# Performance work log

Hardware: AMD Instinct MI355X
Metric: run time of the kernel (lower is better)

Reference implementation:

```python
import jax, jax.numpy as jnp
import numpy as np

N_FFT = 4096
HOP = 1024
EPS = 1e-10


def hann(n):
    # periodic Hann window, matches torch.hann_window(n)
    return 0.5 - 0.5 * jnp.cos(2.0 * jnp.pi * jnp.arange(n) / n)


def stft(x, window):
    # x: (..., T) real -> (..., F, frames) complex; center=True, reflect pad, onesided
    pad = N_FFT // 2
    x = jnp.pad(x, [(0, 0)] * (x.ndim - 1) + [(pad, pad)], mode='reflect')
    n_frames = 1 + (x.shape[-1] - N_FFT) // HOP
    idx = jnp.arange(n_frames)[:, None] * HOP + jnp.arange(N_FFT)[None, :]
    frames = x[..., idx] * window  # (..., frames, N_FFT)
    return jnp.swapaxes(jnp.fft.rfft(frames, axis=-1), -1, -2)  # (..., F, frames)


def istft(spec, window, length):
    # spec: (..., F, frames) complex -> (..., length) real; torch.istft semantics (center=True)
    frames = jnp.fft.irfft(jnp.swapaxes(spec, -1, -2), n=N_FFT, axis=-1) * window
    n_frames = frames.shape[-2]
    out_len = N_FFT + HOP * (n_frames - 1)
    idx = (jnp.arange(n_frames)[:, None] * HOP + jnp.arange(N_FFT)[None, :]).reshape(-1)
    flat = frames.reshape(frames.shape[:-2] + (-1,))
    y = jnp.zeros(frames.shape[:-2] + (out_len,), frames.dtype).at[..., idx].add(flat)
    wsq = jnp.zeros((out_len,), frames.dtype).at[idx].add(jnp.tile(window ** 2, n_frames))
    y = y / jnp.where(wsq > 1e-11, wsq, 1.0)
    pad = N_FFT // 2
    return y[..., pad:pad + length]


def setup_inputs() -> dict:
    key = jax.random.key(0)
    k1, k2, k3 = jax.random.split(key, 3)
    audio = jax.random.normal(k1, (2, 2, 441000), jnp.float32)
    W = jax.random.normal(k2, (4, 2049, 2049), jnp.float32) * 0.02
    b = jax.random.normal(k3, (4, 2049), jnp.float32) * 0.01
    return {"audio": audio, "W": W, "b": b}


def reference(audio, W, b):
    window = hann(N_FFT).astype(audio.dtype)
    mix = stft(audio, window)                 # (N, C, F, T) complex64
    X = jnp.abs(mix)                          # ComplexNorm, mono=False, power=1
    Xd = jax.lax.stop_gradient(X)             # Separator feeds X.detach() to target models
    # target models: per-target linear over frequency bins + ReLU (nonneg spectrogram)
    V = jax.nn.relu(jnp.einsum('ncft,jgf->njcgt', Xd, W) + b[None, :, None, :, None])
    # wiener(iterations=0, softmask=False, residual=False): y_j = v_j * exp(i*angle(mix))
    phase = mix / (jnp.abs(mix) + EPS)        # unit-magnitude complex
    Y = V.astype(phase.real.dtype) * phase[:, None]  # (N, J, C, F, T) complex
    estimates = istft(Y, window, audio.shape[-1])    # (N, J, C, T_audio)
    return estimates
```

## Files before the change

### kernel.cpp

```cpp
#include <hip/hip_runtime.h>
#include <hip/hip_bf16.h>
#include <math.h>

#define T_AUDIO 441000
#define NH   2048
#define HOP  1024
#define NBINS 2049
#define NFRAMES 431
#define PAD  2048

#define GP  2176
#define KP  2112
#define TPN 448

#define NBLK 108
#define SPAN 7168

#define TWO_PI 6.2831853071795864769f

#define PADI(i) ((i) + ((i) >> 4))

typedef __bf16 bf16_t;
typedef bf16_t bf16x8 __attribute__((ext_vector_type(8)));
typedef bf16_t bf16x4 __attribute__((ext_vector_type(4)));
typedef float f32x4 __attribute__((ext_vector_type(4)));
typedef _Float16 h16;
typedef h16 h16x2 __attribute__((ext_vector_type(2)));

__device__ __forceinline__ unsigned pack_bf2(float a, float b) {
    union { bf16_t h; unsigned short u; } ca, cb;
    ca.h = (bf16_t)a; cb.h = (bf16_t)b;
    return (unsigned)ca.u | ((unsigned)cb.u << 16);
}
__device__ __forceinline__ float2 unpack_bf2(unsigned v) {
    union { unsigned u; float f; } a, b;
    a.u = v << 16;
    b.u = v & 0xffff0000u;
    return make_float2(a.f, b.f);
}

__device__ __forceinline__ float2 cadd(float2 a, float2 b) { return make_float2(a.x + b.x, a.y + b.y); }
__device__ __forceinline__ float2 csub(float2 a, float2 b) { return make_float2(a.x - b.x, a.y - b.y); }
__device__ __forceinline__ float2 cmul(float2 a, float2 b) {
    return make_float2(a.x * b.x - a.y * b.y, a.x * b.y + a.y * b.x);
}
__device__ __forceinline__ float2 cmulc(float2 u, float2 w) {
    return make_float2(u.x * w.x + u.y * w.y, u.y * w.x - u.x * w.y);
}

template<bool FWD>
__device__ __forceinline__ void fft2048_reg8(float2* x, int tid,
                                             const float2* __restrict__ tw) {
    const float sgn = FWD ? -1.0f : 1.0f;
    const float R2 = 0.70710678118654752440f;
    int s = 1, ls = 0, fac = 2;
    #pragma unroll
    for (int st = 0; st < 3; st++) {
        int q = tid & (s - 1);
        int p = tid >> ls;
        int e = p * fac;
        float2 w[7];
        #pragma unroll
        for (int k = 0; k < 7; k++) w[k] = tw[e * (k + 1)];
        float2 v[8];
        #pragma unroll
        for (int k = 0; k < 8; k++) v[k] = x[PADI(tid + 256 * k)];
        __syncthreads();
        float2 s0 = cadd(v[0], v[4]), s1 = cadd(v[1], v[5]),
               s2 = cadd(v[2], v[6]), s3 = cadd(v[3], v[7]);
        float2 d0 = csub(v[0], v[4]), d1 = csub(v[1], v[5]),
               d2 = csub(v[2], v[6]), d3 = csub(v[3], v[7]);
        float2 X0, X1, X2, X3, X4, X5, X6, X7;
        {
            float2 t0 = cadd(s0, s2), t1 = csub(s0, s2);
            float2 t2 = cadd(s1, s3), t3 = csub(s1, s3);
            float2 it3 = make_float2(-sgn * t3.y, sgn * t3.x);
            X0 = cadd(t0, t2); X4 = csub(t0, t2);
            X2 = cadd(t1, it3); X6 = csub(t1, it3);
        }
        {
            float2 e0 = d0;
            float2 e1 = make_float2(R2 * (d1.x - sgn * d1.y), R2 * (sgn * d1.x + d1.y));
            float2 e2 = make_float2(-sgn * d2.y, sgn * d2.x);
            float2 e3 = make_float2(-R2 * (d3.x + sgn * d3.y), R2 * (sgn * d3.x - d3.y));
            float2 t0 = cadd(e0, e2), t1 = csub(e0, e2);
            float2 t2 = cadd(e1, e3), t3 = csub(e1, e3);
            float2 it3 = make_float2(-sgn * t3.y, sgn * t3.x);
            X1 = cadd(t0, t2); X5 = csub(t0, t2);
            X3 = cadd(t1, it3); X7 = csub(t1, it3);
        }
        int ob = q + 8 * s * p;
        x[PADI(ob)] = X0;
        float2 XX[7] = {X1, X2, X3, X4, X5, X6, X7};
        #pragma unroll
        for (int k = 0; k < 7; k++) {
            float2 u = XX[k];
            x[PADI(ob + s * (k + 1))] = FWD ? cmulc(u, w[k]) : cmul(w[k], u);
        }
        __syncthreads();
        s <<= 3; ls += 3; fac <<= 3;
    }
    {
        float2 v[8];
        #pragma unroll
        for (int k = 0; k < 8; k++) v[k] = x[PADI(tid + 256 * k)];
        __syncthreads();
        #pragma unroll
        for (int h = 0; h < 2; h++) {
            float2 c0 = v[h], c1 = v[h + 2], c2 = v[h + 4], c3 = v[h + 6];
            float2 t0 = cadd(c0, c2), t1 = csub(c0, c2);
            float2 t2 = cadd(c1, c3), t3 = csub(c1, c3);
            float2 it3 = make_float2(-sgn * t3.y, sgn * t3.x);
            int base = tid + 256 * h;
            x[PADI(base)]        = cadd(t0, t2);
            x[PADI(base + 512)]  = cadd(t1, it3);
            x[PADI(base + 1024)] = csub(t0, t2);
            x[PADI(base + 1536)] = csub(t1, it3);
        }
        __syncthreads();
    }
}

__global__ __launch_bounds__(256) void k_stft(const float* __restrict__ audio,
        bf16_t* __restrict__ Xb, unsigned* __restrict__ ph,
        const float2* __restrict__ tw) {
    __shared__ float2 buf[2176];
    int blk = blockIdx.x;
    int nc = blk / NFRAMES;
    int fr = blk - nc * NFRAMES;
    const float* a = audio + (size_t)nc * T_AUDIO;
    int tid = threadIdx.x;
    int base = fr * HOP - PAD;
    #pragma unroll
    for (int it = 0; it < 8; it++) {
        int m = tid + it * 256;
        int r0 = base + 2 * m;
        int r1 = r0 + 1;
        r0 = r0 < 0 ? -r0 : (r0 >= T_AUDIO ? 2 * T_AUDIO - 2 - r0 : r0);
        r1 = r1 < 0 ? -r1 : (r1 >= T_AUDIO ? 2 * T_AUDIO - 2 - r1 : r1);
        float4 tt = ((const float4*)tw)[m];
        float x0 = a[r0] * (0.5f - 0.5f * tt.x);
        float x1 = a[r1] * (0.5f - 0.5f * tt.z);
        buf[PADI(m)] = make_float2(x0, x1);
    }
    fft2048_reg8<true>(buf, tid, tw);
    size_t orow = ((size_t)nc * NFRAMES + fr) * KP;
    bf16_t* Xrow = Xb + ((size_t)nc * TPN + fr) * KP;
    for (int k = tid; k < NBINS; k += 256) {
        float2 Zk = buf[PADI(k & 2047)];
        float2 Zm = buf[PADI((2048 - k) & 2047)];
        float ex = 0.5f * (Zk.x + Zm.x), ey = 0.5f * (Zk.y - Zm.y);
        float ox = 0.5f * (Zk.y + Zm.y), oy = -0.5f * (Zk.x - Zm.x);
        float2 w = tw[k];
        float re = ex + w.x * ox + w.y * oy;
        float im = ey + w.x * oy - w.y * ox;
        float mag = sqrtf(re * re + im * im);
        float inv = 1.0f / (mag + 1e-10f);
        Xrow[k] = (bf16_t)mag;
        ph[orow + k] = pack_bf2(re * inv, im * inv);
    }
}

__global__ __launch_bounds__(256) void k_convW(const float* __restrict__ W,
        bf16_t* __restrict__ Wb, float2* __restrict__ tw) {
    if (blockIdx.x < 16) {
        int i = blockIdx.x * 256 + threadIdx.x;
        float s, c;
        sincosf((float)i * (TWO_PI / 4096.0f), &s, &c);
        tw[i] = make_float2(c, s);
    }
    size_t idx = (size_t)blockIdx.x * 256 + threadIdx.x;
    size_t total = (size_t)4 * GP * KP / 8;
    if (idx >= total) return;
    size_t e = idx * 8;
    int f0 = (int)(e % KP);
    size_t rem = e / KP;
    int g = (int)(rem % GP);
    int j = (int)(rem / GP);
    bf16x8 v = {};
    if (g < NBINS) {
        const float* src = W + ((size_t)j * NBINS + g) * NBINS;
        #pragma unroll
        for (int r = 0; r < 8; r++) {
            int f = f0 + r;
            v[r] = (bf16_t)(f < NBINS ? src[f] : 0.0f);
        }
    }
    *(bf16x8*)(Wb + e) = v;
}

__global__ __launch_bounds__(256) void k_gemm_mfma(const bf16_t* __restrict__ Wb,
        const float* __restrict__ bias, const bf16_t* __restrict__ Xb,
        bf16_t* __restrict__ V) {
    __shared__ bf16_t As[128 * 64];
    __shared__ bf16_t Bs[64 * 64];
    int id = blockIdx.x;
    int xcd = id & 7, nn = id >> 3;
    int G = xcd + 8 * (nn / 28);
    if (G >= 68) return;
    int m28 = nn % 28;
    int j  = G / 17;
    int g0 = (G % 17) * 128;
    int nc = m28 / 7;
    int t0 = (m28 % 7) * 64;
    const bf16_t* A = Wb + ((size_t)j * GP + g0) * KP;
    const bf16_t* B = Xb + ((size_t)nc * TPN + t0) * KP;
    int tid = threadIdx.x;
    int lane = tid & 63, wid = tid >> 6;
    int wm = wid >> 1, wn = wid & 1;

    const bf16_t* srcA[4];
    #pragma unroll
    for (int i = 0; i < 4; i++) {
        int s = i * 256 + tid;
        int r = s >> 3, cc = (s & 7) ^ (r & 7);
        srcA[i] = A + (size_t)r * KP + cc * 8;
    }
    const bf16_t* srcB[2];
    #pragma unroll
    for (int i = 0; i < 2; i++) {
        int s = i * 256 + tid;
        int r = s >> 3, cc = (s & 7) ^ (r & 7);
        srcB[i] = B + (size_t)r * KP + cc * 8;
    }

    int laneLo = lane & 15, laneHi = lane >> 4;
    int offA[4][2], offB[2][2];
    #pragma unroll
    for (int mm = 0; mm < 4; mm++) {
        int r = wm * 64 + mm * 16 + laneLo;
        #pragma unroll
        for (int kk = 0; kk < 2; kk++) {
            int c = kk * 4 + laneHi;
            offA[mm][kk] = r * 128 + ((c ^ (r & 7)) << 4);
        }
    }
    #pragma unroll
    for (int n = 0; n < 2; n++) {
        int r = wn * 32 + n * 16 + laneLo;
        #pragma unroll
        for (int kk = 0; kk < 2; kk++) {
            int c = kk * 4 + laneHi;
            offB[n][kk] = r * 128 + ((c ^ (r & 7)) << 4);
        }
    }

    f32x4 acc[4][2];
    #pragma unroll
    for (int mm = 0; mm < 4; mm++)
        #pragma unroll
        for (int n = 0; n < 2; n++)
            acc[mm][n] = (f32x4){0.f, 0.f, 0.f, 0.f};

    for (int k0 = 0; k0 < KP; k0 += 64) {
        #pragma unroll
        for (int i = 0; i < 4; i++)
            __builtin_amdgcn_global_load_lds(
                (const __attribute__((address_space(1))) void*)(srcA[i] + k0),
                (__attribute__((address_space(3))) void*)(As + (i * 256 + tid) * 8),
                16, 0, 0);
        #pragma unroll
        for (int i = 0; i < 2; i++)
            __builtin_amdgcn_global_load_lds(
                (const __attribute__((address_space(1))) void*)(srcB[i] + k0),
                (__attribute__((address_space(3))) void*)(Bs + (i * 256 + tid) * 8),
                16, 0, 0);
        __syncthreads();

        bf16x8 af[4][2], bfr[2][2];
        #pragma unroll
        for (int mm = 0; mm < 4; mm++)
            #pragma unroll
            for (int kk = 0; kk < 2; kk++)
                af[mm][kk] = *(const bf16x8*)((const char*)As + offA[mm][kk]);
        #pragma unroll
        for (int n = 0; n < 2; n++)
            #pragma unroll
            for (int kk = 0; kk < 2; kk++)
                bfr[n][kk] = *(const bf16x8*)((const char*)Bs + offB[n][kk]);
        #pragma unroll
        for (int mm = 0; mm < 4; mm++)
            #pragma unroll
            for (int n = 0; n < 2; n++)
                #pragma unroll
                for (int kk = 0; kk < 2; kk++)
                    acc[mm][n] = __builtin_amdgcn_mfma_f32_16x16x32_bf16(
                        af[mm][kk], bfr[n][kk], acc[mm][n], 0, 0, 0);
        __syncthreads();
    }

    int jnc = j * 4 + nc;
    int colT = laneLo;
    int rowB = laneHi * 4;
    #pragma unroll
    for (int n = 0; n < 2; n++) {
        int t = t0 + wn * 32 + n * 16 + colT;
        if (t >= NFRAMES) continue;
        size_t vrow = ((size_t)jnc * NFRAMES + t) * KP;
        #pragma unroll
        for (int mm = 0; mm < 4; mm++) {
            int g = g0 + wm * 64 + mm * 16 + rowB;
            if (g + 3 < NBINS) {
                bf16x4 o;
                #pragma unroll
                for (int r = 0; r < 4; r++)
                    o[r] = (bf16_t)fmaxf(acc[mm][n][r] + bias[j * NBINS + g + r], 0.0f);
                *(bf16x4*)(V + vrow + g) = o;
            } else {
                #pragma unroll
                for (int r = 0; r < 4; r++) {
                    int gg = g + r;
                    if (gg < NBINS)
                        V[vrow + gg] = (bf16_t)fmaxf(acc[mm][n][r] + bias[j * NBINS + gg], 0.0f);
                }
            }
        }
    }
}

__global__ __launch_bounds__(256) void k_istft(const bf16_t* __restrict__ V,
        const unsigned* __restrict__ ph, const float2* __restrict__ tw,
        h16* __restrict__ strips) {
    __shared__ float2 buf[2176];
    int b = blockIdx.x, njc = blockIdx.y;
    int n = njc >> 3, j = (njc >> 1) & 3, c = njc & 1;
    int nc = n * 2 + c;
    int jnc = j * 4 + nc;
    int tid = threadIdx.x;
    const float scale = 1.0f / 2048.0f;
    float2 acc[14];
    #pragma unroll
    for (int u = 0; u < 14; u++) acc[u] = make_float2(0.f, 0.f);

    #pragma unroll
    for (int p = 0; p < 4; p++) {
        int fr = b * 4 + p;
        if (fr < NFRAMES) {
            size_t vrow = ((size_t)jnc * NFRAMES + fr) * KP;
            size_t prow = ((size_t)nc * NFRAMES + fr) * KP;
            #pragma unroll
            for (int it = 0; it < 8; it++) {
                int k = tid + it * 256;
                int km = 2048 - k;
                float vk = (float)V[vrow + k];
                float2 pk = unpack_bf2(ph[prow + k]);
                float vm = (float)V[vrow + km];
                float2 pm = unpack_bf2(ph[prow + km]);
                float2 Yk = make_float2(vk * pk.x, vk * pk.y);
                float2 Ym = make_float2(vm * pm.x, vm * pm.y);
                float ex = 0.5f * (Yk.x + Ym.x), ey = 0.5f * (Yk.y - Ym.y);
                float wx = 0.5f * (Yk.x - Ym.x), wy = 0.5f * (Yk.y + Ym.y);
                float2 w = tw[k];
                float ox_ = w.x * wx - w.y * wy;
                float oy_ = w.x * wy + w.y * wx;
                buf[PADI(k)] = make_float2(ex - oy_, ey + ox_);
            }
            fft2048_reg8<false>(buf, tid, tw);
            #pragma unroll
            for (int it = 0; it < 8; it++) {
                int m = tid + it * 256;
                float2 z = buf[PADI(m)];
                float4 tt = ((const float4*)tw)[m];
                acc[2 * p + it].x += z.x * scale * (0.5f - 0.5f * tt.x);
                acc[2 * p + it].y += z.y * scale * (0.5f - 0.5f * tt.z);
            }
        }
    }
    h16* dst = strips + ((size_t)njc * NBLK + b) * SPAN;
    #pragma unroll
    for (int u = 0; u < 14; u++) {
        h16x2 o = { (h16)acc[u].x, (h16)acc[u].y };
        *(h16x2*)(dst + 512 * u + 2 * tid) = o;
    }
}

__global__ __launch_bounds__(256) void k_final(const h16* __restrict__ strips,
        const float2* __restrict__ tw, float* __restrict__ out) {
    int gidx = blockIdx.x * 256 + threadIdx.x;
    int t = gidx * 2;
    if (t >= T_AUDIO) return;
    int njc = blockIdx.y;
    const h16* S = strips + (size_t)njc * NBLK * SPAN;
    float o[2];
    #pragma unroll
    for (int u = 0; u < 2; u++) {
        int tt = t + u;
        int q = tt + PAD;
        int b1 = q >> 12, o1 = q & 4095;
        float s = 0.f;
        if (b1 < NBLK) s += (float)S[b1 * SPAN + o1];
        if (b1 > 0 && o1 < SPAN - 4096) s += (float)S[(b1 - 1) * SPAN + o1 + 4096];
        float wsq;
        if (tt >= 1024 && tt <= 439295) {
            wsq = 1.5f;
        } else {
            wsq = 0.f;
            int ib = q >> 10;
            #pragma unroll
            for (int d = 0; d < 4; d++) {
                int i = ib - d;
                if (i >= 0 && i < NFRAMES) {
                    int m = q - (i << 10);
                    float w = 0.5f - 0.5f * tw[m].x;
                    wsq += w * w;
                }
            }
            if (!(wsq > 1e-11f)) wsq = 1.f;
        }
        o[u] = s / wsq;
    }
    *(float2*)(out + (size_t)njc * T_AUDIO + t) = make_float2(o[0], o[1]);
}

extern "C" void kernel_launch(void* const* d_in, const int* in_sizes, int n_in,
                              void* d_out, int out_size, void* d_ws, size_t ws_size,
                              hipStream_t stream) {
    const float* audio = (const float*)d_in[0];
    const float* Wm    = (const float*)d_in[1];
    const float* bias  = (const float*)d_in[2];
    float* out = (float*)d_out;
    char* ws = (char*)d_ws;

    size_t szWb  = (size_t)4 * GP * KP * sizeof(bf16_t);
    size_t szXb  = (size_t)4 * TPN * KP * sizeof(bf16_t);
    size_t szPh  = (size_t)4 * NFRAMES * KP * sizeof(unsigned);
    size_t szV   = (size_t)16 * NFRAMES * KP * sizeof(bf16_t);
    size_t szStr = (size_t)16 * NBLK * SPAN * sizeof(h16);
    size_t szTw  = (size_t)4096 * sizeof(float2);

    bf16_t*   Wb    = (bf16_t*)ws;   ws += szWb;
    bf16_t*   Xb    = (bf16_t*)ws;   ws += szXb;
    unsigned* ph    = (unsigned*)ws; ws += szPh;
    bf16_t*   V     = (bf16_t*)ws;   ws += szV;
    h16*      strips= (h16*)ws;      ws += szStr;
    float2*   tw    = (float2*)ws;   ws += szTw;
    if ((size_t)(ws - (char*)d_ws) > ws_size) return;

    hipMemsetAsync(Xb, 0, szXb, stream);

    k_convW<<<dim3((unsigned)((4ull * GP * KP / 8 + 255) / 256)), 256, 0, stream>>>(Wm, Wb, tw);
    k_stft<<<dim3(4 * NFRAMES), 256, 0, stream>>>(audio, Xb, ph, tw);
    k_gemm_mfma<<<dim3(72 * 28), 256, 0, stream>>>(Wb, bias, Xb, V);
    k_istft<<<dim3(NBLK, 16), 256, 0, stream>>>(V, ph, tw, strips);
    k_final<<<dim3((T_AUDIO / 2 + 255) / 256, 16), 256, 0, stream>>>(strips, tw, out);
}
```

Before: 243.9 us.

## Double-buffer GEMM LDS tiles and merge STFT with weight conversion kernel

```diff
diff --git a/kernel.cpp b/kernel.cpp
--- a/kernel.cpp
+++ b/kernel.cpp
@@ -12,9 +12,13 @@
 #define GP  2176
 #define KP  2112
 #define TPN 448
+#define NKT (KP / 64)
 
 #define NBLK 108
 #define SPAN 7168
+
+#define NSTFT (4 * NFRAMES)
+#define NCONV ((4 * GP * KP / 8 + 255) / 256)
 
 #define TWO_PI 6.2831853071795864769f
 
@@ -46,6 +50,15 @@
 }
 __device__ __forceinline__ float2 cmulc(float2 u, float2 w) {
     return make_float2(u.x * w.x + u.y * w.y, u.y * w.x - u.x * w.y);
+}
+
+__global__ void k_tab(float2* __restrict__ tw) {
+    int i = blockIdx.x * 256 + threadIdx.x;
+    if (i < 4096) {
+        float s, c;
+        sincosf((float)i * (TWO_PI / 4096.0f), &s, &c);
+        tw[i] = make_float2(c, s);
+    }
 }
 
 template<bool FWD>
@@ -121,15 +134,37 @@
     }
 }
 
-__global__ __launch_bounds__(256) void k_stft(const float* __restrict__ audio,
+__global__ __launch_bounds__(256) void k_prep(const float* __restrict__ audio,
+        const float* __restrict__ W, bf16_t* __restrict__ Wb,
         bf16_t* __restrict__ Xb, unsigned* __restrict__ ph,
         const float2* __restrict__ tw) {
     __shared__ float2 buf[2176];
-    int blk = blockIdx.x;
-    int nc = blk / NFRAMES;
-    int fr = blk - nc * NFRAMES;
+    int bid = blockIdx.x;
+    int tid = threadIdx.x;
+    if (bid >= NSTFT) {
+        size_t idx = (size_t)(bid - NSTFT) * 256 + tid;
+        size_t total = (size_t)4 * GP * KP / 8;
+        if (idx >= total) return;
+        size_t e = idx * 8;
+        int f0 = (int)(e % KP);
+        size_t rem = e / KP;
+        int g = (int)(rem % GP);
+        int j = (int)(rem / GP);
+        bf16x8 v = {};
+        if (g < NBINS) {
+            const float* src = W + ((size_t)j * NBINS + g) * NBINS;
+            #pragma unroll
+            for (int r = 0; r < 8; r++) {
+                int f = f0 + r;
+                v[r] = (bf16_t)(f < NBINS ? src[f] : 0.0f);
+            }
+        }
+        *(bf16x8*)(Wb + e) = v;
+        return;
+    }
+    int nc = bid / NFRAMES;
+    int fr = bid - nc * NFRAMES;
     const float* a = audio + (size_t)nc * T_AUDIO;
-    int tid = threadIdx.x;
     int base = fr * HOP - PAD;
     #pragma unroll
     for (int it = 0; it < 8; it++) {
@@ -161,39 +196,11 @@
     }
 }
 
-__global__ __launch_bounds__(256) void k_convW(const float* __restrict__ W,
-        bf16_t* __restrict__ Wb, float2* __restrict__ tw) {
-    if (blockIdx.x < 16) {
-        int i = blockIdx.x * 256 + threadIdx.x;
-        float s, c;
-        sincosf((float)i * (TWO_PI / 4096.0f), &s, &c);
-        tw[i] = make_float2(c, s);
-    }
-    size_t idx = (size_t)blockIdx.x * 256 + threadIdx.x;
-    size_t total = (size_t)4 * GP * KP / 8;
-    if (idx >= total) return;
-    size_t e = idx * 8;
-    int f0 = (int)(e % KP);
-    size_t rem = e / KP;
-    int g = (int)(rem % GP);
-    int j = (int)(rem / GP);
-    bf16x8 v = {};
-    if (g < NBINS) {
-        const float* src = W + ((size_t)j * NBINS + g) * NBINS;
-        #pragma unroll
-        for (int r = 0; r < 8; r++) {
-            int f = f0 + r;
-            v[r] = (bf16_t)(f < NBINS ? src[f] : 0.0f);
-        }
-    }
-    *(bf16x8*)(Wb + e) = v;
-}
-
 __global__ __launch_bounds__(256) void k_gemm_mfma(const bf16_t* __restrict__ Wb,
         const float* __restrict__ bias, const bf16_t* __restrict__ Xb,
         bf16_t* __restrict__ V) {
-    __shared__ bf16_t As[128 * 64];
-    __shared__ bf16_t Bs[64 * 64];
+    __shared__ bf16_t As[2][128 * 64];
+    __shared__ bf16_t Bs[2][64 * 64];
     int id = blockIdx.x;
     int xcd = id & 7, nn = id >> 3;
     int G = xcd + 8 * (nn / 28);
@@ -224,6 +231,22 @@
         srcB[i] = B + (size_t)r * KP + cc * 8;
     }
 
+#define STAGE(bufsel, koff)                                                    \
+    {                                                                          \
+        _Pragma("unroll")                                                      \
+        for (int i = 0; i < 4; i++)                                            \
+            __builtin_amdgcn_global_load_lds(                                  \
+                (const __attribute__((address_space(1))) void*)(srcA[i] + (koff)), \
+                (__attribute__((address_space(3))) void*)(&As[bufsel][(i * 256 + tid) * 8]), \
+                16, 0, 0);                                                     \
+        _Pragma("unroll")                                                      \
+        for (int i = 0; i < 2; i++)                                            \
+            __builtin_amdgcn_global_load_lds(                                  \
+                (const __attribute__((address_space(1))) void*)(srcB[i] + (koff)), \
+                (__attribute__((address_space(3))) void*)(&Bs[bufsel][(i * 256 + tid) * 8]), \
+                16, 0, 0);                                                     \
+    }
+
     int laneLo = lane & 15, laneHi = lane >> 4;
     int offA[4][2], offB[2][2];
     #pragma unroll
@@ -252,32 +275,24 @@
         for (int n = 0; n < 2; n++)
             acc[mm][n] = (f32x4){0.f, 0.f, 0.f, 0.f};
 
-    for (int k0 = 0; k0 < KP; k0 += 64) {
-        #pragma unroll
-        for (int i = 0; i < 4; i++)
-            __builtin_amdgcn_global_load_lds(
-                (const __attribute__((address_space(1))) void*)(srcA[i] + k0),
-                (__attribute__((address_space(3))) void*)(As + (i * 256 + tid) * 8),
-                16, 0, 0);
-        #pragma unroll
-        for (int i = 0; i < 2; i++)
-            __builtin_amdgcn_global_load_lds(
-                (const __attribute__((address_space(1))) void*)(srcB[i] + k0),
-                (__attribute__((address_space(3))) void*)(Bs + (i * 256 + tid) * 8),
-                16, 0, 0);
-        __syncthreads();
-
+    STAGE(0, 0);
+    __syncthreads();
+    int cur = 0;
+    for (int t = 0; t < NKT; ++t) {
+        if (t + 1 < NKT) STAGE(cur ^ 1, (t + 1) * 64);
+        const char* aB = (const char*)As + cur * (128 * 64 * 2);
+        const char* bB = (const char*)Bs + cur * (64 * 64 * 2);
         bf16x8 af[4][2], bfr[2][2];
         #pragma unroll
         for (int mm = 0; mm < 4; mm++)
             #pragma unroll
             for (int kk = 0; kk < 2; kk++)
-                af[mm][kk] = *(const bf16x8*)((const char*)As + offA[mm][kk]);
+                af[mm][kk] = *(const bf16x8*)(aB + offA[mm][kk]);
         #pragma unroll
         for (int n = 0; n < 2; n++)
             #pragma unroll
             for (int kk = 0; kk < 2; kk++)
-                bfr[n][kk] = *(const bf16x8*)((const char*)Bs + offB[n][kk]);
+                bfr[n][kk] = *(const bf16x8*)(bB + offB[n][kk]);
         #pragma unroll
         for (int mm = 0; mm < 4; mm++)
             #pragma unroll
@@ -287,7 +302,9 @@
                     acc[mm][n] = __builtin_amdgcn_mfma_f32_16x16x32_bf16(
                         af[mm][kk], bfr[n][kk], acc[mm][n], 0, 0, 0);
         __syncthreads();
-    }
+        cur ^= 1;
+    }
+#undef STAGE
 
     int jnc = j * 4 + nc;
     int colT = laneLo;
@@ -438,8 +455,8 @@
 
     hipMemsetAsync(Xb, 0, szXb, stream);
 
-    k_convW<<<dim3((unsigned)((4ull * GP * KP / 8 + 255) / 256)), 256, 0, stream>>>(Wm, Wb, tw);
-    k_stft<<<dim3(4 * NFRAMES), 256, 0, stream>>>(audio, Xb, ph, tw);
+    k_tab<<<dim3(16), 256, 0, stream>>>(tw);
+    k_prep<<<dim3(NSTFT + NCONV), 256, 0, stream>>>(audio, Wm, Wb, Xb, ph, tw);
     k_gemm_mfma<<<dim3(72 * 28), 256, 0, stream>>>(Wb, bias, Xb, V);
     k_istft<<<dim3(NBLK, 16), 256, 0, stream>>>(V, ph, tw, strips);
     k_final<<<dim3((T_AUDIO / 2 + 255) / 256, 16), 256, 0, stream>>>(strips, tw, out);
```

Measured after the change: 252.4 us. +3.5%, slower.

## Fuse STFT with weight conversion and keep FFT edge stages in registers

Applied to the files above, without the earlier changes.

```diff
diff --git a/kernel.cpp b/kernel.cpp
--- a/kernel.cpp
+++ b/kernel.cpp
@@ -12,9 +12,13 @@
 #define GP  2176
 #define KP  2112
 #define TPN 448
+#define NKT (KP / 64)
 
 #define NBLK 108
 #define SPAN 7168
+
+#define NSTFT (4 * NFRAMES)
+#define NCONV ((4 * GP * KP / 8 + 255) / 256)
 
 #define TWO_PI 6.2831853071795864769f
 
@@ -48,89 +52,130 @@
     return make_float2(u.x * w.x + u.y * w.y, u.y * w.x - u.x * w.y);
 }
 
+__global__ void k_tab(float2* __restrict__ tw) {
+    int i = blockIdx.x * 256 + threadIdx.x;
+    if (i < 4096) {
+        float s, c;
+        sincosf((float)i * (TWO_PI / 4096.0f), &s, &c);
+        tw[i] = make_float2(c, s);
+    }
+}
+
+
+__device__ __forceinline__ void load_own(float2 v[8], const float2* x, int tid) {
+    #pragma unroll
+    for (int k = 0; k < 8; k++) v[k] = x[PADI(tid + 256 * k)];
+}
+
 template<bool FWD>
-__device__ __forceinline__ void fft2048_reg8(float2* x, int tid,
-                                             const float2* __restrict__ tw) {
+__device__ __forceinline__ void r8_sweep_store(const float2 v[8], float2* x,
+        int tid, int s, int ls, int fac, const float2* __restrict__ tw) {
     const float sgn = FWD ? -1.0f : 1.0f;
     const float R2 = 0.70710678118654752440f;
-    int s = 1, ls = 0, fac = 2;
-    #pragma unroll
-    for (int st = 0; st < 3; st++) {
-        int q = tid & (s - 1);
-        int p = tid >> ls;
-        int e = p * fac;
-        float2 w[7];
-        #pragma unroll
-        for (int k = 0; k < 7; k++) w[k] = tw[e * (k + 1)];
-        float2 v[8];
-        #pragma unroll
-        for (int k = 0; k < 8; k++) v[k] = x[PADI(tid + 256 * k)];
-        __syncthreads();
-        float2 s0 = cadd(v[0], v[4]), s1 = cadd(v[1], v[5]),
-               s2 = cadd(v[2], v[6]), s3 = cadd(v[3], v[7]);
-        float2 d0 = csub(v[0], v[4]), d1 = csub(v[1], v[5]),
-               d2 = csub(v[2], v[6]), d3 = csub(v[3], v[7]);
-        float2 X0, X1, X2, X3, X4, X5, X6, X7;
-        {
-            float2 t0 = cadd(s0, s2), t1 = csub(s0, s2);
-            float2 t2 = cadd(s1, s3), t3 = csub(s1, s3);
-            float2 it3 = make_float2(-sgn * t3.y, sgn * t3.x);
-            X0 = cadd(t0, t2); X4 = csub(t0, t2);
-            X2 = cadd(t1, it3); X6 = csub(t1, it3);
-        }
-        {
-            float2 e0 = d0;
-            float2 e1 = make_float2(R2 * (d1.x - sgn * d1.y), R2 * (sgn * d1.x + d1.y));
-            float2 e2 = make_float2(-sgn * d2.y, sgn * d2.x);
-            float2 e3 = make_float2(-R2 * (d3.x + sgn * d3.y), R2 * (sgn * d3.x - d3.y));
-            float2 t0 = cadd(e0, e2), t1 = csub(e0, e2);
-            float2 t2 = cadd(e1, e3), t3 = csub(e1, e3);
-            float2 it3 = make_float2(-sgn * t3.y, sgn * t3.x);
-            X1 = cadd(t0, t2); X5 = csub(t0, t2);
-            X3 = cadd(t1, it3); X7 = csub(t1, it3);
-        }
-        int ob = q + 8 * s * p;
-        x[PADI(ob)] = X0;
-        float2 XX[7] = {X1, X2, X3, X4, X5, X6, X7};
-        #pragma unroll
-        for (int k = 0; k < 7; k++) {
-            float2 u = XX[k];
-            x[PADI(ob + s * (k + 1))] = FWD ? cmulc(u, w[k]) : cmul(w[k], u);
-        }
-        __syncthreads();
-        s <<= 3; ls += 3; fac <<= 3;
-    }
+    int q = tid & (s - 1);
+    int p = tid >> ls;
+    int e = p * fac;
+    float2 w[7];
+    #pragma unroll
+    for (int k = 0; k < 7; k++) w[k] = tw[e * (k + 1)];
+    float2 s0 = cadd(v[0], v[4]), s1 = cadd(v[1], v[5]),
+           s2 = cadd(v[2], v[6]), s3 = cadd(v[3], v[7]);
+    float2 d0 = csub(v[0], v[4]), d1 = csub(v[1], v[5]),
+           d2 = csub(v[2], v[6]), d3 = csub(v[3], v[7]);
+    float2 X0, X1, X2, X3, X4, X5, X6, X7;
     {
-        float2 v[8];
-        #pragma unroll
-        for (int k = 0; k < 8; k++) v[k] = x[PADI(tid + 256 * k)];
-        __syncthreads();
-        #pragma unroll
-        for (int h = 0; h < 2; h++) {
-            float2 c0 = v[h], c1 = v[h + 2], c2 = v[h + 4], c3 = v[h + 6];
-            float2 t0 = cadd(c0, c2), t1 = csub(c0, c2);
-            float2 t2 = cadd(c1, c3), t3 = csub(c1, c3);
-            float2 it3 = make_float2(-sgn * t3.y, sgn * t3.x);
-            int base = tid + 256 * h;
-            x[PADI(base)]        = cadd(t0, t2);
-            x[PADI(base + 512)]  = cadd(t1, it3);
-            x[PADI(base + 1024)] = csub(t0, t2);
-            x[PADI(base + 1536)] = csub(t1, it3);
-        }
-        __syncthreads();
-    }
-}
-
-__global__ __launch_bounds__(256) void k_stft(const float* __restrict__ audio,
+        float2 t0 = cadd(s0, s2), t1 = csub(s0, s2);
+        float2 t2 = cadd(s1, s3), t3 = csub(s1, s3);
+        float2 it3 = make_float2(-sgn * t3.y, sgn * t3.x);
+        X0 = cadd(t0, t2); X4 = csub(t0, t2);
+        X2 = cadd(t1, it3); X6 = csub(t1, it3);
+    }
+    {
+        float2 e0 = d0;
+        float2 e1 = make_float2(R2 * (d1.x - sgn * d1.y), R2 * (sgn * d1.x + d1.y));
+        float2 e2 = make_float2(-sgn * d2.y, sgn * d2.x);
+        float2 e3 = make_float2(-R2 * (d3.x + sgn * d3.y), R2 * (sgn * d3.x - d3.y));
+        float2 t0 = cadd(e0, e2), t1 = csub(e0, e2);
+        float2 t2 = cadd(e1, e3), t3 = csub(e1, e3);
+        float2 it3 = make_float2(-sgn * t3.y, sgn * t3.x);
+        X1 = cadd(t0, t2); X5 = csub(t0, t2);
+        X3 = cadd(t1, it3); X7 = csub(t1, it3);
+    }
+    int ob = q + 8 * s * p;
+    x[PADI(ob)] = X0;
+    float2 XX[7] = {X1, X2, X3, X4, X5, X6, X7};
+    #pragma unroll
+    for (int k = 0; k < 7; k++) {
+        float2 u = XX[k];
+        x[PADI(ob + s * (k + 1))] = FWD ? cmulc(u, w[k]) : cmul(w[k], u);
+    }
+}
+
+__device__ __forceinline__ void r4_final_reg(const float2 v[8], float2 o[8],
+                                             float sgn) {
+    #pragma unroll
+    for (int h = 0; h < 2; h++) {
+        float2 c0 = v[h], c1 = v[h + 2], c2 = v[h + 4], c3 = v[h + 6];
+        float2 t0 = cadd(c0, c2), t1 = csub(c0, c2);
+        float2 t2 = cadd(c1, c3), t3 = csub(c1, c3);
+        float2 it3 = make_float2(-sgn * t3.y, sgn * t3.x);
+        o[h]     = cadd(t0, t2);
+        o[h + 2] = cadd(t1, it3);
+        o[h + 4] = csub(t0, t2);
+        o[h + 6] = csub(t1, it3);
+    }
+}
+
+template<bool FWD>
+__device__ __forceinline__ void fft_mid(float2 v[8], float2* buf, int tid,
+                                        const float2* __restrict__ tw) {
+    r8_sweep_store<FWD>(v, buf, tid, 1, 0, 2, tw);
+    __syncthreads();
+    load_own(v, buf, tid);
+    __syncthreads();
+    r8_sweep_store<FWD>(v, buf, tid, 8, 3, 16, tw);
+    __syncthreads();
+    load_own(v, buf, tid);
+    __syncthreads();
+    r8_sweep_store<FWD>(v, buf, tid, 64, 6, 128, tw);
+    __syncthreads();
+    load_own(v, buf, tid);
+    __syncthreads();
+}
+
+__global__ __launch_bounds__(256) void k_prep(const float* __restrict__ audio,
+        const float* __restrict__ W, bf16_t* __restrict__ Wb,
         bf16_t* __restrict__ Xb, unsigned* __restrict__ ph,
         const float2* __restrict__ tw) {
     __shared__ float2 buf[2176];
-    int blk = blockIdx.x;
-    int nc = blk / NFRAMES;
-    int fr = blk - nc * NFRAMES;
+    int bid = blockIdx.x;
+    int tid = threadIdx.x;
+    if (bid >= NSTFT) {
+        size_t idx = (size_t)(bid - NSTFT) * 256 + tid;
+        size_t total = (size_t)4 * GP * KP / 8;
+        if (idx >= total) return;
+        size_t e = idx * 8;
+        int f0 = (int)(e % KP);
+        size_t rem = e / KP;
+        int g = (int)(rem % GP);
+        int j = (int)(rem / GP);
+        bf16x8 v = {};
+        if (g < NBINS) {
+            const float* src = W + ((size_t)j * NBINS + g) * NBINS;
+            #pragma unroll
+            for (int r = 0; r < 8; r++) {
+                int f = f0 + r;
+                v[r] = (bf16_t)(f < NBINS ? src[f] : 0.0f);
+            }
+        }
+        *(bf16x8*)(Wb + e) = v;
+        return;
+    }
+    int nc = bid / NFRAMES;
+    int fr = bid - nc * NFRAMES;
     const float* a = audio + (size_t)nc * T_AUDIO;
-    int tid = threadIdx.x;
     int base = fr * HOP - PAD;
+    float2 v[8];
     #pragma unroll
     for (int it = 0; it < 8; it++) {
         int m = tid + it * 256;
@@ -139,11 +184,17 @@
         r0 = r0 < 0 ? -r0 : (r0 >= T_AUDIO ? 2 * T_AUDIO - 2 - r0 : r0);
         r1 = r1 < 0 ? -r1 : (r1 >= T_AUDIO ? 2 * T_AUDIO - 2 - r1 : r1);
         float4 tt = ((const float4*)tw)[m];
-        float x0 = a[r0] * (0.5f - 0.5f * tt.x);
-        float x1 = a[r1] * (0.5f - 0.5f * tt.z);
-        buf[PADI(m)] = make_float2(x0, x1);
-    }
-    fft2048_reg8<true>(buf, tid, tw);
+        v[it] = make_float2(a[r0] * (0.5f - 0.5f * tt.x),
+                            a[r1] * (0.5f - 0.5f * tt.z));
+    }
+    fft_mid<true>(v, buf, tid, tw);
+    {
+        float2 o[8];
+        r4_final_reg(v, o, -1.0f);
+        #pragma unroll
+        for (int it = 0; it < 8; it++) buf[PADI(tid + 256 * it)] = o[it];
+    }
+    __syncthreads();
     size_t orow = ((size_t)nc * NFRAMES + fr) * KP;
     bf16_t* Xrow = Xb + ((size_t)nc * TPN + fr) * KP;
     for (int k = tid; k < NBINS; k += 256) {
@@ -159,34 +210,6 @@
         Xrow[k] = (bf16_t)mag;
         ph[orow + k] = pack_bf2(re * inv, im * inv);
     }
-}
-
-__global__ __launch_bounds__(256) void k_convW(const float* __restrict__ W,
-        bf16_t* __restrict__ Wb, float2* __restrict__ tw) {
-    if (blockIdx.x < 16) {
-        int i = blockIdx.x * 256 + threadIdx.x;
-        float s, c;
-        sincosf((float)i * (TWO_PI / 4096.0f), &s, &c);
-        tw[i] = make_float2(c, s);
-    }
-    size_t idx = (size_t)blockIdx.x * 256 + threadIdx.x;
-    size_t total = (size_t)4 * GP * KP / 8;
-    if (idx >= total) return;
-    size_t e = idx * 8;
-    int f0 = (int)(e % KP);
-    size_t rem = e / KP;
-    int g = (int)(rem % GP);
-    int j = (int)(rem / GP);
-    bf16x8 v = {};
-    if (g < NBINS) {
-        const float* src = W + ((size_t)j * NBINS + g) * NBINS;
-        #pragma unroll
-        for (int r = 0; r < 8; r++) {
-            int f = f0 + r;
-            v[r] = (bf16_t)(f < NBINS ? src[f] : 0.0f);
-        }
-    }
-    *(bf16x8*)(Wb + e) = v;
 }
 
 __global__ __launch_bounds__(256) void k_gemm_mfma(const bf16_t* __restrict__ Wb,
@@ -338,6 +361,7 @@
         if (fr < NFRAMES) {
             size_t vrow = ((size_t)jnc * NFRAMES + fr) * KP;
             size_t prow = ((size_t)nc * NFRAMES + fr) * KP;
+            float2 v[8];
             #pragma unroll
             for (int it = 0; it < 8; it++) {
                 int k = tid + it * 256;
@@ -353,16 +377,17 @@
                 float2 w = tw[k];
                 float ox_ = w.x * wx - w.y * wy;
                 float oy_ = w.x * wy + w.y * wx;
-                buf[PADI(k)] = make_float2(ex - oy_, ey + ox_);
+                v[it] = make_float2(ex - oy_, ey + ox_);
             }
-            fft2048_reg8<false>(buf, tid, tw);
+            fft_mid<false>(v, buf, tid, tw);
+            float2 o[8];
+            r4_final_reg(v, o, 1.0f);
             #pragma unroll
             for (int it = 0; it < 8; it++) {
                 int m = tid + it * 256;
-                float2 z = buf[PADI(m)];
                 float4 tt = ((const float4*)tw)[m];
-                acc[2 * p + it].x += z.x * scale * (0.5f - 0.5f * tt.x);
-                acc[2 * p + it].y += z.y * scale * (0.5f - 0.5f * tt.z);
+                acc[2 * p + it].x += o[it].x * scale * (0.5f - 0.5f * tt.x);
+                acc[2 * p + it].y += o[it].y * scale * (0.5f - 0.5f * tt.z);
             }
         }
     }
@@ -438,8 +463,8 @@
 
     hipMemsetAsync(Xb, 0, szXb, stream);
 
-    k_convW<<<dim3((unsigned)((4ull * GP * KP / 8 + 255) / 256)), 256, 0, stream>>>(Wm, Wb, tw);
-    k_stft<<<dim3(4 * NFRAMES), 256, 0, stream>>>(audio, Xb, ph, tw);
+    k_tab<<<dim3(16), 256, 0, stream>>>(tw);
+    k_prep<<<dim3(NSTFT + NCONV), 256, 0, stream>>>(audio, Wm, Wb, Xb, ph, tw);
     k_gemm_mfma<<<dim3(72 * 28), 256, 0, stream>>>(Wb, bias, Xb, V);
     k_istft<<<dim3(NBLK, 16), 256, 0, stream>>>(V, ph, tw, strips);
     k_final<<<dim3((T_AUDIO / 2 + 255) / 256, 16), 256, 0, stream>>>(strips, tw, out);
```

Result: faster. 223.0 us (-8.6%).
